# Kernel optimization log

Hardware: AMD Instinct MI355X
Metric: run time of the kernel (lower is better)

Reference implementation:

```python
import math
import jax, jax.numpy as jnp
import numpy as np

C1, D, NUM_HEADS, K_CH = 150, 32, 4, 10
GLOBAL_TOPK_RATIO = 0.08


def _pos2d(h, w, dim):
    d2 = dim // 2
    div = jnp.exp(jnp.arange(0, d2, 2, dtype=jnp.float32) * (-(math.log(10000.0) / d2)))
    def axis_pe(n):
        ang = jnp.arange(n, dtype=jnp.float32)[:, None] * div[None, :]
        pe = jnp.zeros((n, d2), dtype=jnp.float32)
        pe = pe.at[:, 0::2].set(jnp.sin(ang))
        pe = pe.at[:, 1::2].set(jnp.cos(ang))
        return pe
    pe_y = axis_pe(h)  # [h, d2]
    pe_x = axis_pe(w)  # [w, d2]
    return jnp.concatenate([
        jnp.broadcast_to(pe_y[:, None, :], (h, w, d2)),
        jnp.broadcast_to(pe_x[None, :, :], (h, w, d2)),
    ], axis=-1)  # [h, w, dim]


def setup_inputs() -> dict:
    key = jax.random.key(0)
    ks = jax.random.split(key, 7)
    B = 1024
    return {
        "x": jax.random.uniform(ks[0], (B, 1, 28, 28), dtype=jnp.float32),
        "conv1_w": jax.random.normal(ks[1], (C1, 1, 9, 9), dtype=jnp.float32) * 0.05,
        "channel_embed": jax.random.normal(ks[2], (C1, D), dtype=jnp.float32) * 0.02,
        "in_proj_w": jax.random.normal(ks[3], (3 * D, D), dtype=jnp.float32) * (1.0 / math.sqrt(D)),
        "in_proj_b": jnp.zeros((3 * D,), dtype=jnp.float32),
        "out_proj_w": jax.random.normal(ks[4], (D, D), dtype=jnp.float32) * (1.0 / math.sqrt(D)),
        "out_proj_b": jnp.zeros((D,), dtype=jnp.float32),
    }


def reference(x, conv1_w, channel_embed, in_proj_w, in_proj_b, out_proj_w, out_proj_b):
    # conv1 + relu: [B,1,28,28] -> [B,150,14,14]
    A = jax.nn.relu(jax.lax.conv_general_dilated(
        x, conv1_w, window_strides=(2, 2), padding=((4, 4), (4, 4)),
        dimension_numbers=("NCHW", "OIHW", "NCHW")))
    B, C, H, W = A.shape
    total = C * H * W
    k_global = max(1, int(math.ceil(GLOBAL_TOPK_RATIO * total)))
    A_flat = A.reshape(B, -1)
    # global kthvalue threshold: k_global-th largest per sample
    thresh = jax.lax.top_k(A_flat, k_global)[0][:, -1:]
    A_global = (A_flat * (A_flat >= thresh)).reshape(B, C, H, W)
    # per-location channel top-k + scatter
    v = jnp.transpose(A_global, (0, 2, 3, 1))  # [B,H,W,C]
    topv, topi = jax.lax.top_k(v, K_CH)        # [B,H,W,k]
    N = B * H * W
    logits = jnp.zeros((N, C), v.dtype).at[
        jnp.arange(N)[:, None], topi.reshape(N, K_CH)
    ].set(topv.reshape(N, K_CH)).reshape(v.shape)
    # normalize by per-sample global max (guard zero)
    flat_logits = logits.reshape(B, -1)
    gmax = jnp.max(flat_logits, axis=1, keepdims=True)
    normed = jnp.where(gmax == 0, 0.0, flat_logits / jnp.where(gmax == 0, 1.0, gmax))
    sparse_weights = normed.reshape(logits.shape)  # [B,H,W,C]
    # channel embedding + 2D sinusoidal PE
    loc_emb = jnp.einsum("bhwc,cd->bhwd", sparse_weights, channel_embed)
    loc_emb = loc_emb + _pos2d(H, W, D)[None]
    seq = loc_emb.reshape(B, H * W, D)
    # 1-layer MHA (self-attention, batch_first)
    qkv = seq @ in_proj_w.T + in_proj_b  # [B,S,3D]
    q, k, vv = jnp.split(qkv, 3, axis=-1)
    hd = D // NUM_HEADS
    def heads(t):
        return jnp.transpose(t.reshape(B, H * W, NUM_HEADS, hd), (0, 2, 1, 3))
    q, k, vv = heads(q), heads(k), heads(vv)
    attn = jax.nn.softmax(jnp.einsum("bnsd,bntd->bnst", q, k) / math.sqrt(hd), axis=-1)
    ctx = jnp.einsum("bnst,bntd->bnsd", attn, vv)
    ctx = jnp.transpose(ctx, (0, 2, 1, 3)).reshape(B, H * W, D)
    attn_out = ctx @ out_proj_w.T + out_proj_b  # [B, 196, 32]
    return attn_out
```

## Files before the change

kernel.cpp:

```cpp
#include <hip/hip_runtime.h>
#include <math.h>

#define NC1 150
#define HW 196
#define NB 1024
#define DD 32
#define NHD 4
#define HDIM 8
#define KG 2352
#define KCH 10
#define CAP 48
#define CVS 49
#define CES 36
#define KVS 20

typedef float v2f __attribute__((ext_vector_type(2)));

__device__ __forceinline__ float dot32v(const v2f* __restrict__ xr2,
                                        const float* __restrict__ wr, float bias) {
  const float4* w4 = (const float4*)wr;
  v2f s0 = {bias, 0.f};
  v2f s1 = {0.f, 0.f};
#pragma unroll
  for (int e = 0; e < 8; ++e) {
    float4 w = w4[e];
    v2f wlo = {w.x, w.y}, whi = {w.z, w.w};
    s0 = __builtin_elementwise_fma(xr2[2 * e], wlo, s0);
    s1 = __builtin_elementwise_fma(xr2[2 * e + 1], whi, s1);
  }
  v2f s = s0 + s1;
  return s.x + s.y;
}

#define UNI_F 17552
#define XT_OFF 0
#define WT_OFF 8232
#define CV_OFF 0
#define CC_OFF 9604
#define CNT_OFF 11956
#define CE_OFF 12152

__global__ void prep2_kernel(const float* __restrict__ cw, float* __restrict__ wtg,
                             float* __restrict__ pos) {
  int i = blockIdx.x * 256 + threadIdx.x;
  if (i < HW * DD) {
    int s = i >> 5, d = i & 31;
    int h = s / 14, w = s % 14;
    int p = (d < 16) ? h : w;
    int dd = (d < 16) ? d : d - 16;
    int j = dd >> 1;
    float dv = expf(-(logf(10000.0f) / 16.0f) * (float)(2 * j));
    float ang = (float)p * dv;
    pos[i] = (dd & 1) ? cosf(ang) : sinf(ang);
    return;
  }
  int j = i - HW * DD;
  if (j < 84 * 152) {
    int k = j / 152, c = j - k * 152;
    wtg[j] = (k < 81 && c < NC1) ? cw[c * 81 + k] : 0.f;
  }
}

__global__ __launch_bounds__(1024, 8) void fused_kernel(const float* __restrict__ x,
                                                        const float* __restrict__ wtg,
                                                        const float* __restrict__ CE,
                                                        const float* __restrict__ pos,
                                                        float* __restrict__ seqo) {
  __shared__ alignas(16) float uni[UNI_F];
  __shared__ alignas(16) float xs[784];
  __shared__ unsigned hist[2048];
  __shared__ unsigned wsum[4];
  __shared__ unsigned s_prefix, s_krem, s_max;

  int b = blockIdx.x, tid = threadIdx.x;
  int lane = tid & 63, wid = tid >> 6;

  if (tid < 196) ((float4*)xs)[tid] = ((const float4*)(x + (size_t)b * 784))[tid];
  if (tid == 0) { s_prefix = 0u; s_krem = KG; s_max = 0u; }
  __syncthreads();

  int cg = tid / 49;
  int g  = tid - cg * 49;
  bool act = (tid < 931);
  float acc[4][8];
#pragma unroll
  for (int i = 0; i < 4; ++i)
#pragma unroll
    for (int j = 0; j < 8; ++j) acc[i][j] = 0.f;

  float* XT = uni + XT_OFF;
  float* WT = uni + WT_OFF;

  for (int kb = 0; kb < 84; kb += 42) {
    for (int i = tid; i < 42 * 196; i += 1024) {
      int kk = i / 196, s = i - kk * 196;
      int k = kb + kk;
      float v = 0.f;
      if (k < 81) {
        int ki = k / 9, kj = k - ki * 9;
        int h = s / 14, w = s - h * 14;
        int r = 2 * h - 4 + ki, c = 2 * w - 4 + kj;
        if (r >= 0 && r < 28 && c >= 0 && c < 28) v = xs[r * 28 + c];
      }
      XT[i] = v;
    }
    for (int i = tid; i < (42 * 152) / 4; i += 1024)
      ((float4*)WT)[i] = ((const float4*)(wtg + kb * 152))[i];
    __syncthreads();
    if (act) {
      const float* xtp = XT + 4 * g;
      const float* wtp = WT + 8 * cg;
#pragma unroll 7
      for (int kk = 0; kk < 42; ++kk) {
        float4 xv = *(const float4*)(xtp + kk * 196);
        float4 w0 = *(const float4*)(wtp + kk * 152);
        float4 w1 = *(const float4*)(wtp + kk * 152 + 4);
        float xa[4] = {xv.x, xv.y, xv.z, xv.w};
        float wa[8] = {w0.x, w0.y, w0.z, w0.w, w1.x, w1.y, w1.z, w1.w};
#pragma unroll
        for (int i = 0; i < 4; ++i)
#pragma unroll
          for (int j = 0; j < 8; ++j) acc[i][j] += xa[i] * wa[j];
      }
    }
    __syncthreads();
  }

#pragma unroll
  for (int i = 0; i < 4; ++i)
#pragma unroll
    for (int j = 0; j < 8; ++j) acc[i][j] = fmaxf(acc[i][j], 0.f);

  for (int pass = 0; pass < 3; ++pass) {
    hist[tid] = 0u; hist[tid + 1024] = 0u;
    __syncthreads();
    int shift = (pass == 0) ? 21 : (pass == 1 ? 10 : 0);
    int bits = (pass == 2) ? 10 : 11;
    unsigned mask = (1u << bits) - 1u;
    unsigned pfx = s_prefix;
    unsigned krem = s_krem;
    int hishift = shift + bits;
    if (pass == 0) {
      unsigned mymax = 0u;
#pragma unroll
      for (int i = 0; i < 4; ++i)
#pragma unroll
        for (int j = 0; j < 8; ++j) {
          unsigned u = __float_as_uint(acc[i][j]);
          mymax = max(mymax, u);
          if (u) atomicAdd(&hist[u >> 21], 1u);
        }
#pragma unroll
      for (int st = 32; st >= 1; st >>= 1)
        mymax = max(mymax, (unsigned)__shfl_xor((int)mymax, st));
      if (lane == 0) atomicMax(&s_max, mymax);
    } else {
#pragma unroll
      for (int i = 0; i < 4; ++i)
#pragma unroll
        for (int j = 0; j < 8; ++j) {
          unsigned u = __float_as_uint(acc[i][j]);
          if (u && (u >> hishift) == pfx) atomicAdd(&hist[(u >> shift) & mask], 1u);
        }
    }
    __syncthreads();
    int segsz = (1 << bits) >> 8;
    unsigned segv = 0u, sufv = 0u;
    if (tid < 256) {
      for (int j = 0; j < segsz; ++j) segv += hist[tid * segsz + j];
      sufv = segv;
#pragma unroll
      for (int st = 1; st < 64; st <<= 1) {
        unsigned o = (unsigned)__shfl_down((int)sufv, st);
        if (lane + st < 64) sufv += o;
      }
      if (lane == 0) wsum[wid] = sufv;
    }
    __syncthreads();
    if (tid < 256) {
      unsigned tail = 0u;
      for (int ww = wid + 1; ww < 4; ++ww) tail += wsum[ww];
      sufv += tail;
      unsigned above = sufv - segv;
      if (above < krem && sufv >= krem) {
        unsigned cum = above;
        int dsel = tid * segsz;
        for (int d2 = segsz - 1; d2 >= 0; --d2) {
          int dd = tid * segsz + d2;
          if (cum + hist[dd] >= krem) { dsel = dd; break; }
          cum += hist[dd];
        }
        s_prefix = (pfx << bits) | (unsigned)dsel;
        s_krem = krem - cum;
      }
    }
    __syncthreads();
  }

  float* candV = uni + CV_OFF;
  unsigned char* candC = (unsigned char*)(uni + CC_OFF);
  unsigned* cnt = (unsigned*)(uni + CNT_OFF);
  if (tid < 196) cnt[tid] = 0u;
  __syncthreads();
  float T = __uint_as_float(s_prefix);
  if (act) {
#pragma unroll
    for (int i = 0; i < 4; ++i) {
      int loc = 4 * g + i;
#pragma unroll
      for (int j = 0; j < 8; ++j) {
        float v = acc[i][j];
        if (v >= T && v > 0.f) {
          unsigned slot = atomicAdd(&cnt[loc], 1u);
          if (slot < CAP) {
            candV[loc * CVS + slot] = v;
            candC[loc * CAP + slot] = (unsigned char)(8 * cg + j);
          }
        }
      }
    }
  }
  __syncthreads();

  float* CEs = uni + CE_OFF;
  if (tid >= 196) {
    for (int i = tid - 196; i < NC1 * 32; i += 1024 - 196) {
      int c = i >> 5, e = i & 31;
      CEs[c * CES + e] = CE[i];
    }
  }
  float tv[KCH]; int tc[KCH];
  if (tid < 196) {
    int loc = tid;
    unsigned n = cnt[loc]; if (n > CAP) n = CAP;
#pragma unroll
    for (int k = 0; k < KCH; ++k) { tv[k] = 0.f; tc[k] = 0; }
    for (unsigned jj = 0; jj < n; ++jj) {
      float v = candV[loc * CVS + jj];
      int c = candC[loc * CAP + jj];
      if (v > tv[KCH - 1] || (v == tv[KCH - 1] && c < tc[KCH - 1])) {
        float iv = v; int ic = c;
#pragma unroll
        for (int j = 0; j < KCH; ++j) {
          bool gt = (iv > tv[j]) || (iv == tv[j] && ic < tc[j]);
          float nv = gt ? iv : tv[j]; int nc = gt ? ic : tc[j];
          float ov = gt ? tv[j] : iv; int oc = gt ? tc[j] : ic;
          tv[j] = nv; tc[j] = nc; iv = ov; ic = oc;
        }
      }
    }
  }
  __syncthreads();

  if (tid < 196) {
    float gm = __uint_as_float(s_max);
    float gi = (gm == 0.0f) ? 0.0f : 1.0f / gm;
    float acc2[32];
#pragma unroll
    for (int e = 0; e < 32; ++e) acc2[e] = 0.f;
#pragma unroll
    for (int k = 0; k < KCH; ++k) {
      float v = tv[k];
      const float4* cr = (const float4*)(CEs + tc[k] * CES);
#pragma unroll
      for (int e4 = 0; e4 < 8; ++e4) {
        float4 cv = cr[e4];
        acc2[e4 * 4 + 0] += v * cv.x;
        acc2[e4 * 4 + 1] += v * cv.y;
        acc2[e4 * 4 + 2] += v * cv.z;
        acc2[e4 * 4 + 3] += v * cv.w;
      }
    }
    float* op = seqo + ((size_t)b * HW + tid) * DD;
    const float* pr = pos + tid * DD;
#pragma unroll
    for (int e4 = 0; e4 < 8; ++e4) {
      float4 pv = ((const float4*)pr)[e4];
      float4 o;
      o.x = acc2[e4 * 4 + 0] * gi + pv.x;
      o.y = acc2[e4 * 4 + 1] * gi + pv.y;
      o.z = acc2[e4 * 4 + 2] * gi + pv.z;
      o.w = acc2[e4 * 4 + 3] * gi + pv.w;
      ((float4*)op)[e4] = o;
    }
  }
}

__global__ __launch_bounds__(832, 3) void attn_kernel(const float* __restrict__ seq,
                                                      const float* __restrict__ Wqkv,
                                                      const float* __restrict__ bqkv,
                                                      float* __restrict__ ctxo) {
  __shared__ alignas(16) float kvs[NHD * HW * KVS];
  __shared__ alignas(16) float swq[96 * DD];
  __shared__ float sbq[96];
  __shared__ unsigned s_kk[NHD];

  int b = blockIdx.x, tid = threadIdx.x;
  int h = tid / HW;
  int s = tid - h * HW;
  bool act = (tid < NHD * HW);

  float xr[32];
  if (act) {
    const float* row = seq + ((size_t)b * HW + s) * DD;
#pragma unroll
    for (int e = 0; e < 8; ++e) {
      float4 f = ((const float4*)row)[e];
      xr[e * 4 + 0] = f.x; xr[e * 4 + 1] = f.y; xr[e * 4 + 2] = f.z; xr[e * 4 + 3] = f.w;
    }
  }
  for (int i = tid; i < (96 * DD) / 4; i += 832)
    ((float4*)swq)[i] = ((const float4*)Wqkv)[i];
  if (tid < 96) sbq[tid] = bqkv[tid];
  if (tid < NHD) s_kk[tid] = 0u;
  __syncthreads();

  float q[8]; float qq = 0.f;
  if (act) {
    float* kvrow = kvs + (h * HW + s) * KVS;
    {
      float ka[8]; float kk = 0.f;
#pragma unroll
      for (int d = 0; d < 8; ++d) {
        const float* wr = swq + (32 + h * HDIM + d) * DD;
        float acc = sbq[32 + h * HDIM + d];
#pragma unroll
        for (int e = 0; e < DD; e += 4) {
          float4 wv = *(const float4*)(wr + e);
          acc += xr[e + 0] * wv.x + xr[e + 1] * wv.y + xr[e + 2] * wv.z + xr[e + 3] * wv.w;
        }
        ka[d] = acc; kk += acc * acc;
      }
      float4 k0 = {ka[0], ka[1], ka[2], ka[3]}, k1 = {ka[4], ka[5], ka[6], ka[7]};
      ((float4*)kvrow)[0] = k0; ((float4*)kvrow)[1] = k1;
      atomicMax(&s_kk[h], __float_as_uint(kk));
    }
    {
      float va[8];
#pragma unroll
      for (int d = 0; d < 8; ++d) {
        const float* wr = swq + (64 + h * HDIM + d) * DD;
        float acc = sbq[64 + h * HDIM + d];
#pragma unroll
        for (int e = 0; e < DD; e += 4) {
          float4 wv = *(const float4*)(wr + e);
          acc += xr[e + 0] * wv.x + xr[e + 1] * wv.y + xr[e + 2] * wv.z + xr[e + 3] * wv.w;
        }
        va[d] = acc;
      }
      float4 v0 = {va[0], va[1], va[2], va[3]}, v1 = {va[4], va[5], va[6], va[7]};
      ((float4*)kvrow)[2] = v0; ((float4*)kvrow)[3] = v1;
    }
#pragma unroll
    for (int d = 0; d < 8; ++d) {
      const float* wr = swq + (h * HDIM + d) * DD;
      float acc = sbq[h * HDIM + d];
#pragma unroll
      for (int e = 0; e < DD; e += 4) {
        float4 wv = *(const float4*)(wr + e);
        acc += xr[e + 0] * wv.x + xr[e + 1] * wv.y + xr[e + 2] * wv.z + xr[e + 3] * wv.w;
      }
      q[d] = acc; qq += acc * acc;
    }
  }
  __syncthreads();
  if (!act) return;

  const float scale = 0.3535533905932738f;
  float kkmax = __uint_as_float(s_kk[h]);
  float negM = -sqrtf(qq * kkmax) * scale;
  float l = 0.f;
  float c0 = 0.f, c1 = 0.f, c2 = 0.f, c3 = 0.f, c4 = 0.f, c5 = 0.f, c6 = 0.f, c7 = 0.f;
  const float4* kp = (const float4*)(kvs + (h * HW) * KVS);
#pragma unroll 4
  for (int t = 0; t < HW; ++t) {
    float4 k0 = kp[0], k1 = kp[1], v0 = kp[2], v1 = kp[3];
    kp += 5;
    float sc = q[0] * k0.x;
    sc = fmaf(q[1], k0.y, sc); sc = fmaf(q[2], k0.z, sc); sc = fmaf(q[3], k0.w, sc);
    sc = fmaf(q[4], k1.x, sc); sc = fmaf(q[5], k1.y, sc); sc = fmaf(q[6], k1.z, sc);
    sc = fmaf(q[7], k1.w, sc);
    float p = __expf(fmaf(sc, scale, negM));
    l += p;
    c0 = fmaf(p, v0.x, c0); c1 = fmaf(p, v0.y, c1); c2 = fmaf(p, v0.z, c2);
    c3 = fmaf(p, v0.w, c3); c4 = fmaf(p, v1.x, c4); c5 = fmaf(p, v1.y, c5);
    c6 = fmaf(p, v1.z, c6); c7 = fmaf(p, v1.w, c7);
  }
  float inv = 1.0f / l;
  float* op = ctxo + ((size_t)b * HW + s) * DD + h * HDIM;
  float4 o0, o1;
  o0.x = c0 * inv; o0.y = c1 * inv; o0.z = c2 * inv; o0.w = c3 * inv;
  o1.x = c4 * inv; o1.y = c5 * inv; o1.z = c6 * inv; o1.w = c7 * inv;
  ((float4*)op)[0] = o0; ((float4*)op)[1] = o1;
}

__global__ __launch_bounds__(256) void outproj_kernel(const float* __restrict__ ctx,
                                                      const float* __restrict__ Wo,
                                                      const float* __restrict__ bo,
                                                      float* __restrict__ out) {
  __shared__ float sw[32 * 32];
  __shared__ float sb2[32];
  int tid = threadIdx.x;
  for (int i = tid; i < 1024; i += 256) sw[i] = Wo[i];
  if (tid < 32) sb2[tid] = bo[tid];
  __syncthreads();
  size_t row = (size_t)blockIdx.x * 256 + tid;
  const float* cr = ctx + row * 32;
  v2f xr2[16];
#pragma unroll
  for (int e = 0; e < 8; ++e) {
    float4 f = ((const float4*)cr)[e];
    v2f lo = {f.x, f.y}, hi = {f.z, f.w};
    xr2[2 * e] = lo; xr2[2 * e + 1] = hi;
  }
  float* op = out + row * 32;
#pragma unroll
  for (int d4 = 0; d4 < 8; ++d4) {
    float4 o;
    float* oo = (float*)&o;
#pragma unroll
    for (int q = 0; q < 4; ++q) {
      int d = d4 * 4 + q;
      oo[q] = dot32v(xr2, sw + d * 32, sb2[d]);
    }
    ((float4*)op)[d4] = o;
  }
}

extern "C" void kernel_launch(void* const* d_in, const int* in_sizes, int n_in,
                              void* d_out, int out_size, void* d_ws, size_t ws_size,
                              hipStream_t stream) {
  const float* x  = (const float*)d_in[0];
  const float* cw = (const float*)d_in[1];
  const float* ce = (const float*)d_in[2];
  const float* wq = (const float*)d_in[3];
  const float* bq = (const float*)d_in[4];
  const float* wo = (const float*)d_in[5];
  const float* bo = (const float*)d_in[6];
  float* out = (float*)d_out;
  float* ws  = (float*)d_ws;

  float* ctx = ws;
  float* pos = ws + (size_t)NB * HW * DD;
  float* wtg = pos + HW * DD;

  prep2_kernel<<<(HW * DD + 84 * 152 + 255) / 256, 256, 0, stream>>>(cw, wtg, pos);
  fused_kernel<<<NB, 1024, 0, stream>>>(x, wtg, ce, pos, out);
  attn_kernel<<<NB, 832, 0, stream>>>(out, wq, bq, ctx);
  outproj_kernel<<<(NB * HW * DD) / (256 * 32), 256, 0, stream>>>(ctx, wo, bo, out);
}
```

Measured before the change: 379.5 us.

## Fuse output projection into attention kernel via shared-memory context tile

Removes the separate outproj kernel. The attention kernel now writes its per-head context into shared memory (reusing the K/V buffer), loads Wo and the bias into the reused weight buffer, and has each thread compute its head's 8 output columns for its row. This avoids writing the full context tensor to global memory, reading it back, and paying one kernel launch. The cost is two extra block barriers and some extra work in the attention kernel. The input seq and the output alias the same buffer, which looks safe because each block reads its seq rows before it writes them, but both pointers are still declared __restrict__.

After: 378.6 us. No clear change (-0.2%).

```diff
diff --git a/kernel.cpp b/kernel.cpp
--- a/kernel.cpp
+++ b/kernel.cpp
@@ -13,24 +13,7 @@
 #define CVS 49
 #define CES 36
 #define KVS 20
-
-typedef float v2f __attribute__((ext_vector_type(2)));
-
-__device__ __forceinline__ float dot32v(const v2f* __restrict__ xr2,
-                                        const float* __restrict__ wr, float bias) {
-  const float4* w4 = (const float4*)wr;
-  v2f s0 = {bias, 0.f};
-  v2f s1 = {0.f, 0.f};
-#pragma unroll
-  for (int e = 0; e < 8; ++e) {
-    float4 w = w4[e];
-    v2f wlo = {w.x, w.y}, whi = {w.z, w.w};
-    s0 = __builtin_elementwise_fma(xr2[2 * e], wlo, s0);
-    s1 = __builtin_elementwise_fma(xr2[2 * e + 1], whi, s1);
-  }
-  v2f s = s0 + s1;
-  return s.x + s.y;
-}
+#define CXS 36
 
 #define UNI_F 17552
 #define XT_OFF 0
@@ -289,7 +272,9 @@
 __global__ __launch_bounds__(832, 3) void attn_kernel(const float* __restrict__ seq,
                                                       const float* __restrict__ Wqkv,
                                                       const float* __restrict__ bqkv,
-                                                      float* __restrict__ ctxo) {
+                                                      const float* __restrict__ Wo,
+                                                      const float* __restrict__ bo,
+                                                      float* __restrict__ outp) {
   __shared__ alignas(16) float kvs[NHD * HW * KVS];
   __shared__ alignas(16) float swq[96 * DD];
   __shared__ float sbq[96];
@@ -364,66 +349,68 @@
     }
   }
   __syncthreads();
-  if (!act) return;
-
-  const float scale = 0.3535533905932738f;
-  float kkmax = __uint_as_float(s_kk[h]);
-  float negM = -sqrtf(qq * kkmax) * scale;
+
   float l = 0.f;
   float c0 = 0.f, c1 = 0.f, c2 = 0.f, c3 = 0.f, c4 = 0.f, c5 = 0.f, c6 = 0.f, c7 = 0.f;
-  const float4* kp = (const float4*)(kvs + (h * HW) * KVS);
+  if (act) {
+    const float scale = 0.3535533905932738f;
+    float kkmax = __uint_as_float(s_kk[h]);
+    float negM = -sqrtf(qq * kkmax) * scale;
+    const float4* kp = (const float4*)(kvs + (h * HW) * KVS);
 #pragma unroll 4
-  for (int t = 0; t < HW; ++t) {
-    float4 k0 = kp[0], k1 = kp[1], v0 = kp[2], v1 = kp[3];
-    kp += 5;
-    float sc = q[0] * k0.x;
-    sc = fmaf(q[1], k0.y, sc); sc = fmaf(q[2], k0.z, sc); sc = fmaf(q[3], k0.w, sc);
-    sc = fmaf(q[4], k1.x, sc); sc = fmaf(q[5], k1.y, sc); sc = fmaf(q[6], k1.z, sc);
-    sc = fmaf(q[7], k1.w, sc);
-    float p = __expf(fmaf(sc, scale, negM));
-    l += p;
-    c0 = fmaf(p, v0.x, c0); c1 = fmaf(p, v0.y, c1); c2 = fmaf(p, v0.z, c2);
-    c3 = fmaf(p, v0.w, c3); c4 = fmaf(p, v1.x, c4); c5 = fmaf(p, v1.y, c5);
-    c6 = fmaf(p, v1.z, c6); c7 = fmaf(p, v1.w, c7);
-  }
-  float inv = 1.0f / l;
-  float* op = ctxo + ((size_t)b * HW + s) * DD + h * HDIM;
-  float4 o0, o1;
-  o0.x = c0 * inv; o0.y = c1 * inv; o0.z = c2 * inv; o0.w = c3 * inv;
-  o1.x = c4 * inv; o1.y = c5 * inv; o1.z = c6 * inv; o1.w = c7 * inv;
-  ((float4*)op)[0] = o0; ((float4*)op)[1] = o1;
-}
-
-__global__ __launch_bounds__(256) void outproj_kernel(const float* __restrict__ ctx,
-                                                      const float* __restrict__ Wo,
-                                                      const float* __restrict__ bo,
-                                                      float* __restrict__ out) {
-  __shared__ float sw[32 * 32];
-  __shared__ float sb2[32];
-  int tid = threadIdx.x;
-  for (int i = tid; i < 1024; i += 256) sw[i] = Wo[i];
-  if (tid < 32) sb2[tid] = bo[tid];
-  __syncthreads();
-  size_t row = (size_t)blockIdx.x * 256 + tid;
-  const float* cr = ctx + row * 32;
-  v2f xr2[16];
-#pragma unroll
-  for (int e = 0; e < 8; ++e) {
-    float4 f = ((const float4*)cr)[e];
-    v2f lo = {f.x, f.y}, hi = {f.z, f.w};
-    xr2[2 * e] = lo; xr2[2 * e + 1] = hi;
-  }
-  float* op = out + row * 32;
-#pragma unroll
-  for (int d4 = 0; d4 < 8; ++d4) {
-    float4 o;
-    float* oo = (float*)&o;
-#pragma unroll
-    for (int q = 0; q < 4; ++q) {
-      int d = d4 * 4 + q;
-      oo[q] = dot32v(xr2, sw + d * 32, sb2[d]);
-    }
-    ((float4*)op)[d4] = o;
+    for (int t = 0; t < HW; ++t) {
+      float4 k0 = kp[0], k1 = kp[1], v0 = kp[2], v1 = kp[3];
+      kp += 5;
+      float sc = q[0] * k0.x;
+      sc = fmaf(q[1], k0.y, sc); sc = fmaf(q[2], k0.z, sc); sc = fmaf(q[3], k0.w, sc);
+      sc = fmaf(q[4], k1.x, sc); sc = fmaf(q[5], k1.y, sc); sc = fmaf(q[6], k1.z, sc);
+      sc = fmaf(q[7], k1.w, sc);
+      float p = __expf(fmaf(sc, scale, negM));
+      l += p;
+      c0 = fmaf(p, v0.x, c0); c1 = fmaf(p, v0.y, c1); c2 = fmaf(p, v0.z, c2);
+      c3 = fmaf(p, v0.w, c3); c4 = fmaf(p, v1.x, c4); c5 = fmaf(p, v1.y, c5);
+      c6 = fmaf(p, v1.z, c6); c7 = fmaf(p, v1.w, c7);
+    }
+  }
+  __syncthreads();
+
+  float* cx = kvs;
+  if (act) {
+    float inv = 1.0f / l;
+    float* cr = cx + s * CXS + h * HDIM;
+    float4 o0 = {c0 * inv, c1 * inv, c2 * inv, c3 * inv};
+    float4 o1 = {c4 * inv, c5 * inv, c6 * inv, c7 * inv};
+    ((float4*)cr)[0] = o0; ((float4*)cr)[1] = o1;
+  }
+  for (int i = tid; i < 256; i += 832)
+    ((float4*)swq)[i] = ((const float4*)Wo)[i];
+  if (tid < 32) sbq[tid] = bo[tid];
+  __syncthreads();
+
+  if (act) {
+    float4 c[8];
+    const float4* crow = (const float4*)(cx + s * CXS);
+#pragma unroll
+    for (int e = 0; e < 8; ++e) c[e] = crow[e];
+    float* op = outp + ((size_t)b * HW + s) * DD + h * HDIM;
+#pragma unroll
+    for (int dq = 0; dq < 2; ++dq) {
+      float4 o;
+      float* oo = (float*)&o;
+#pragma unroll
+      for (int qd = 0; qd < 4; ++qd) {
+        int d = h * HDIM + dq * 4 + qd;
+        const float4* wr = (const float4*)(swq + d * DD);
+        float a2 = sbq[d];
+#pragma unroll
+        for (int e = 0; e < 8; ++e) {
+          float4 w = wr[e];
+          a2 += c[e].x * w.x + c[e].y * w.y + c[e].z * w.z + c[e].w * w.w;
+        }
+        oo[qd] = a2;
+      }
+      ((float4*)op)[dq] = o;
+    }
   }
 }
 
@@ -440,12 +427,10 @@
   float* out = (float*)d_out;
   float* ws  = (float*)d_ws;
 
-  float* ctx = ws;
-  float* pos = ws + (size_t)NB * HW * DD;
+  float* pos = ws;
   float* wtg = pos + HW * DD;
 
   prep2_kernel<<<(HW * DD + 84 * 152 + 255) / 256, 256, 0, stream>>>(cw, wtg, pos);
   fused_kernel<<<NB, 1024, 0, stream>>>(x, wtg, ce, pos, out);
-  attn_kernel<<<NB, 832, 0, stream>>>(out, wq, bq, ctx);
-  outproj_kernel<<<(NB * HW * DD) / (256 * 32), 256, 0, stream>>>(ctx, wo, bo, out);
+  attn_kernel<<<NB, 832, 0, stream>>>(out, wq, bq, wo, bo, out);
 }
```
